# Optimization experiments

Measured on AMD Instinct MI355X. Metric: run time of the kernel, lower is better.

## Reference

```python
import jax, jax.numpy as jnp
import numpy as np
import math

B, S, D, H, L, V = 1, 2048, 512, 8, 2, 32000
DH = D // H
DFF = 2048
EPS = 1e-6
LN_EPS = 1e-5


def setup_inputs() -> dict:
    key = jax.random.key(0)
    ks = jax.random.split(key, 8)
    s = 0.02
    return {
        "input_ids": jax.random.randint(ks[0], (B, S), 0, V),
        "token_emb": jax.random.normal(ks[1], (V, D), jnp.float32) * s,
        "ln1_scale": jnp.ones((L, D), jnp.float32),
        "ln1_bias": jnp.zeros((L, D), jnp.float32),
        "qkv_w": jax.random.normal(ks[2], (L, D, 3 * D), jnp.float32) * s,
        "out_w": jax.random.normal(ks[3], (L, D, D), jnp.float32) * s,
        "ln2_scale": jnp.ones((L, D), jnp.float32),
        "ln2_bias": jnp.zeros((L, D), jnp.float32),
        "mlp_w1": jax.random.normal(ks[4], (L, D, DFF), jnp.float32) * s,
        "mlp_b1": jnp.zeros((L, DFF), jnp.float32),
        "mlp_w2": jax.random.normal(ks[5], (L, DFF, D), jnp.float32) * s,
        "mlp_b2": jnp.zeros((L, D), jnp.float32),
        "lnf_scale": jnp.ones((D,), jnp.float32),
        "lnf_bias": jnp.zeros((D,), jnp.float32),
        "head_w": jax.random.normal(ks[6], (D, V), jnp.float32) * s,
    }


def layernorm(x, scale, bias):
    mu = jnp.mean(x, axis=-1, keepdims=True)
    var = jnp.mean(jnp.square(x - mu), axis=-1, keepdims=True)
    return (x - mu) * jax.lax.rsqrt(var + LN_EPS) * scale + bias


def feature_map(x):
    return jax.nn.elu(x) + 1.0


def sinusoidal_pe(seq_len, d_model, dtype):
    pos = jnp.arange(seq_len, dtype=jnp.float32)[:, None]
    div = jnp.exp(jnp.arange(0, d_model, 2, dtype=jnp.float32) * (-math.log(10000.0) / d_model))
    pe = jnp.zeros((seq_len, d_model), jnp.float32)
    pe = pe.at[:, 0::2].set(jnp.sin(pos * div))
    pe = pe.at[:, 1::2].set(jnp.cos(pos * div))
    return pe.astype(dtype)


def linear_causal_attn(x, w_qkv, w_out):
    # x: (b, s, d)
    b, s, _ = x.shape
    qkv = x @ w_qkv  # (b, s, 3d)
    q, k, v = jnp.split(qkv, 3, axis=-1)
    split_heads = lambda t: t.reshape(b, s, H, DH).transpose(0, 2, 1, 3)  # (b,h,s,dh)
    q, k, v = split_heads(q), split_heads(k), split_heads(v)
    phi_q = feature_map(q)
    phi_k = feature_map(k)
    k_cum = jnp.cumsum(phi_k, axis=2)                          # (b,h,s,dh)
    kv = jnp.einsum('bhsi,bhsj->bhsij', phi_k, v)              # (b,h,s,dh,dh)
    kv_cum = jnp.cumsum(kv, axis=2)
    numer = jnp.einsum('bhsi,bhsij->bhsj', phi_q, kv_cum)      # (b,h,s,dh)
    denom = jnp.einsum('bhsi,bhsi->bhs', phi_q, k_cum) + EPS
    attn = numer / denom[..., None]
    attn = attn.transpose(0, 2, 1, 3).reshape(b, s, D)
    return attn @ w_out


def reference(input_ids, token_emb, ln1_scale, ln1_bias, qkv_w, out_w,
              ln2_scale, ln2_bias, mlp_w1, mlp_b1, mlp_w2, mlp_b2,
              lnf_scale, lnf_bias, head_w):
    tok = token_emb[input_ids]                 # (b, s, d)
    pos = sinusoidal_pe(input_ids.shape[1], D, tok.dtype)[None]
    x = tok + pos
    for l in range(L):
        a = linear_causal_attn(layernorm(x, ln1_scale[l], ln1_bias[l]), qkv_w[l], out_w[l])
        x = x + a
        h = layernorm(x, ln2_scale[l], ln2_bias[l])
        h = jax.nn.gelu(h @ mlp_w1[l] + mlp_b1[l], approximate=False) @ mlp_w2[l] + mlp_b2[l]
        x = x + h
    x = layernorm(x, lnf_scale, lnf_bias)
    logits = x @ head_w                        # (b, s, vocab)
    return logits
```

## Files before the change

### kernel.cpp

```cpp
#include <hip/hip_runtime.h>
#include <cstdint>

typedef unsigned short u16;
typedef __bf16 bf16x8 __attribute__((ext_vector_type(8)));
typedef float f32x4 __attribute__((ext_vector_type(4)));

#define DEV __device__ __forceinline__

DEV u16 f2bf(float f) {
  union { float f; unsigned u; } v; v.f = f;
  unsigned u = v.u;
  u += 0x7FFFu + ((u >> 16) & 1u);
  return (u16)(u >> 16);
}
DEV float bf2f(u16 u) {
  union { unsigned u; float f; } v; v.u = ((unsigned)u) << 16;
  return v.f;
}

DEV void load16(const u16* g, u16* l) {
  __builtin_amdgcn_global_load_lds(
      (const __attribute__((address_space(1))) unsigned int*)(const void*)g,
      (__attribute__((address_space(3))) unsigned int*)l, 16, 0, 0);
}

__global__ __launch_bounds__(256) void prep_kernel(
    const float* __restrict__ qkvw, const float* __restrict__ outw,
    const float* __restrict__ w1, const float* __restrict__ w2,
    const float* __restrict__ hw, u16* __restrict__ wq_t, u16* __restrict__ wo_t,
    u16* __restrict__ w1_t, u16* __restrict__ w2_t, u16* __restrict__ wh_t,
    const int* __restrict__ ids, const float* __restrict__ emb,
    const float* __restrict__ sc, const float* __restrict__ bi,
    float* __restrict__ x, u16* __restrict__ xn) {
  int b = blockIdx.x;
  __shared__ float t[64][65];
  if (b >= 5536) {
    int lane = threadIdx.x & 63, wave = threadIdx.x >> 6;
    int row = (b - 5536) * 4 + wave;
    int id = ids[row];
    float v[8];
#pragma unroll
    for (int i = 0; i < 8; ++i) {
      int c = lane + i * 64;
      float tk = emb[(size_t)id * 512 + c];
      int dp = c & ~1;
      float dv = expf((float)dp * (-9.210340371976184f / 512.0f));
      float ang = (float)row * dv;
      float pe = (c & 1) ? cosf(ang) : sinf(ang);
      v[i] = tk + pe;
      x[(size_t)row * 512 + c] = v[i];
    }
    float s = 0.f;
#pragma unroll
    for (int i = 0; i < 8; ++i) s += v[i];
#pragma unroll
    for (int m = 32; m; m >>= 1) s += __shfl_xor(s, m, 64);
    float mu = s * (1.0f / 512.0f);
    float var = 0.f;
#pragma unroll
    for (int i = 0; i < 8; ++i) { float d = v[i] - mu; var += d * d; }
#pragma unroll
    for (int m = 32; m; m >>= 1) var += __shfl_xor(var, m, 64);
    float rs = rsqrtf(var * (1.0f / 512.0f) + 1e-5f);
    u16* orow = xn + (size_t)row * 512;
#pragma unroll
    for (int i = 0; i < 8; ++i) {
      int c = lane + i * 64;
      orow[c] = f2bf((v[i] - mu) * rs * sc[c] + bi[c]);
    }
    return;
  }
  const float* in; u16* out; int K, N, nx, ky;
  if (b < 384)       { int z = b / 192, r = b % 192; nx = r % 24; ky = r / 24;
                       in = qkvw + (size_t)z * 786432; out = wq_t + (size_t)z * 786432; N = 1536; K = 512; }
  else if (b < 512)  { int tt = b - 384, z = tt / 64, r = tt % 64; nx = r % 8; ky = r / 8;
                       in = outw + (size_t)z * 262144; out = wo_t + (size_t)z * 262144; N = 512; K = 512; }
  else if (b < 1024) { int tt = b - 512, z = tt / 256, r = tt % 256; nx = r % 32; ky = r / 32;
                       in = w1 + (size_t)z * 1048576; out = w1_t + (size_t)z * 1048576; N = 2048; K = 512; }
  else if (b < 1536) { int tt = b - 1024, z = tt / 256, r = tt % 256; nx = r % 8; ky = r / 8;
                       in = w2 + (size_t)z * 1048576; out = w2_t + (size_t)z * 1048576; N = 512; K = 2048; }
  else               { int tt = b - 1536; nx = tt % 500; ky = tt / 500;
                       in = hw; out = wh_t; N = 32000; K = 512; }
  int n0 = nx * 64, k0 = ky * 64;
  for (int e = threadIdx.x; e < 4096; e += 256) {
    int r = e >> 6, c = e & 63;
    t[r][c] = in[(size_t)(k0 + r) * N + n0 + c];
  }
  __syncthreads();
  for (int e = threadIdx.x; e < 4096; e += 256) {
    int r = e >> 6, c = e & 63;
    out[(size_t)(n0 + r) * K + k0 + c] = f2bf(t[c][r]);
  }
}

__global__ __launch_bounds__(256) void reduce_ln(const float* __restrict__ part, int nz,
    const float* __restrict__ bias, float* __restrict__ x,
    const float* __restrict__ sc, const float* __restrict__ bi, u16* __restrict__ xn) {
  int lane = threadIdx.x & 63, wave = threadIdx.x >> 6;
  int row = blockIdx.x * 4 + wave;
  float* xr = x + (size_t)row * 512;
  float v[8];
#pragma unroll
  for (int i = 0; i < 8; ++i) v[i] = xr[lane + i * 64];
  if (bias) {
#pragma unroll
    for (int i = 0; i < 8; ++i) v[i] += bias[lane + i * 64];
  }
  for (int z = 0; z < nz; ++z) {
    const float* pz = part + (size_t)z * 1048576 + (size_t)row * 512;
#pragma unroll
    for (int i = 0; i < 8; ++i) v[i] += pz[lane + i * 64];
  }
#pragma unroll
  for (int i = 0; i < 8; ++i) xr[lane + i * 64] = v[i];
  float s = 0.f;
#pragma unroll
  for (int i = 0; i < 8; ++i) s += v[i];
#pragma unroll
  for (int m = 32; m; m >>= 1) s += __shfl_xor(s, m, 64);
  float mu = s * (1.0f / 512.0f);
  float var = 0.f;
#pragma unroll
  for (int i = 0; i < 8; ++i) { float d = v[i] - mu; var += d * d; }
#pragma unroll
  for (int m = 32; m; m >>= 1) var += __shfl_xor(var, m, 64);
  float rs = rsqrtf(var * (1.0f / 512.0f) + 1e-5f);
  u16* orow = xn + (size_t)row * 512;
#pragma unroll
  for (int i = 0; i < 8; ++i) {
    int c = lane + i * 64;
    orow[c] = f2bf((v[i] - mu) * rs * sc[c] + bi[c]);
  }
}

__global__ __launch_bounds__(256) void attn_intra(const u16* __restrict__ pq,
    const u16* __restrict__ pk, const u16* __restrict__ pv,
    float* __restrict__ numer, float* __restrict__ denom,
    float* __restrict__ KVc, float* __restrict__ Ksc) {
  int c = blockIdx.x, h = blockIdx.y;
  int s0 = c * 128;
  __shared__ u16 kl[128 * 72];
  __shared__ u16 vl[128 * 72];
  __shared__ u16 kT[64 * 136];
  __shared__ u16 vT[64 * 136];
  __shared__ u16 P[128 * 136];
  int tid = threadIdx.x, lane = tid & 63, w = tid >> 6;
  int fr = lane & 15, kb = lane >> 4, rg = lane >> 4;
  const size_t base = ((size_t)h * 2048 + s0) * 64;

  for (int e = tid; e < 1024; e += 256) {
    int r = e >> 3, c8 = (e & 7) * 8;
    *(bf16x8*)&kl[r * 72 + c8] = *(const bf16x8*)&pk[base + r * 64 + c8];
    *(bf16x8*)&vl[r * 72 + c8] = *(const bf16x8*)&pv[base + r * 64 + c8];
  }
  int fiA = w, fiB = 7 - w;
  const u16* qA = pq + base + (size_t)(fiA * 16 + fr) * 64 + kb * 8;
  const u16* qB = pq + base + (size_t)(fiB * 16 + fr) * 64 + kb * 8;
  bf16x8 aQ0a = *(const bf16x8*)qA, aQ1a = *(const bf16x8*)(qA + 32);
  bf16x8 aQ0b = *(const bf16x8*)qB, aQ1b = *(const bf16x8*)(qB + 32);
  __syncthreads();

  {
    int dh = tid & 63, sb = tid >> 6;
#pragma unroll
    for (int b8 = 0; b8 < 4; ++b8) {
      int sbase = sb * 32 + b8 * 8;
      u16 tk[8], tv[8];
#pragma unroll
      for (int j = 0; j < 8; ++j) {
        tk[j] = kl[(sbase + j) * 72 + dh];
        tv[j] = vl[(sbase + j) * 72 + dh];
      }
      *(int4*)&kT[dh * 136 + sbase] = *(const int4*)tk;
      *(int4*)&vT[dh * 136 + sbase] = *(const int4*)tv;
    }
  }

#pragma unroll
  for (int ph = 0; ph < 2; ++ph) {
    int fi = ph ? fiB : fiA;
    bf16x8 aQ0 = ph ? aQ0b : aQ0a, aQ1 = ph ? aQ1b : aQ1a;
    f32x4 dsum = {0.f, 0.f, 0.f, 0.f};
    for (int fj = 0; fj <= fi; ++fj) {
      f32x4 s4 = {0.f, 0.f, 0.f, 0.f};
      bf16x8 b0 = *(const bf16x8*)&kl[(fj * 16 + fr) * 72 + kb * 8];
      bf16x8 b1 = *(const bf16x8*)&kl[(fj * 16 + fr) * 72 + kb * 8 + 32];
      s4 = __builtin_amdgcn_mfma_f32_16x16x32_bf16(aQ0, b0, s4, 0, 0, 0);
      s4 = __builtin_amdgcn_mfma_f32_16x16x32_bf16(aQ1, b1, s4, 0, 0, 0);
      int colL = fj * 16 + fr;
#pragma unroll
      for (int rr = 0; rr < 4; ++rr) {
        int rowL = fi * 16 + rg * 4 + rr;
        float mv = (colL <= rowL) ? s4[rr] : 0.f;
        dsum[rr] += mv;
        P[rowL * 136 + colL] = f2bf(mv);
      }
    }
    if ((fi & 1) == 0) {
      int colL = (fi + 1) * 16 + fr;
#pragma unroll
      for (int rr = 0; rr < 4; ++rr) P[(fi * 16 + rg * 4 + rr) * 136 + colL] = 0;
    }
#pragma unroll
    for (int rr = 0; rr < 4; ++rr) {
      float v = dsum[rr];
      v += __shfl_xor(v, 1, 16); v += __shfl_xor(v, 2, 16);
      v += __shfl_xor(v, 4, 16); v += __shfl_xor(v, 8, 16);
      if (fr == 0) denom[(size_t)h * 2048 + s0 + fi * 16 + rg * 4 + rr] = v;
    }
  }
  __syncthreads();

#pragma unroll
  for (int ph = 0; ph < 2; ++ph) {
    int fi = ph ? fiB : fiA;
    int ktmax = (fi + 2) >> 1;
    f32x4 o0 = {0,0,0,0}, o1 = {0,0,0,0}, o2 = {0,0,0,0}, o3 = {0,0,0,0};
    for (int kt = 0; kt < ktmax; ++kt) {
      bf16x8 aP = *(const bf16x8*)&P[(fi * 16 + fr) * 136 + kt * 32 + kb * 8];
      o0 = __builtin_amdgcn_mfma_f32_16x16x32_bf16(aP, *(const bf16x8*)&vT[(0 * 16 + fr) * 136 + kt * 32 + kb * 8], o0, 0, 0, 0);
      o1 = __builtin_amdgcn_mfma_f32_16x16x32_bf16(aP, *(const bf16x8*)&vT[(1 * 16 + fr) * 136 + kt * 32 + kb * 8], o1, 0, 0, 0);
      o2 = __builtin_amdgcn_mfma_f32_16x16x32_bf16(aP, *(const bf16x8*)&vT[(2 * 16 + fr) * 136 + kt * 32 + kb * 8], o2, 0, 0, 0);
      o3 = __builtin_amdgcn_mfma_f32_16x16x32_bf16(aP, *(const bf16x8*)&vT[(3 * 16 + fr) * 136 + kt * 32 + kb * 8], o3, 0, 0, 0);
    }
#pragma unroll
    for (int rr = 0; rr < 4; ++rr) {
      size_t rb = base + (size_t)(fi * 16 + rg * 4 + rr) * 64;
      numer[rb + 0 + fr]  = o0[rr];
      numer[rb + 16 + fr] = o1[rr];
      numer[rb + 32 + fr] = o2[rr];
      numer[rb + 48 + fr] = o3[rr];
    }
  }

  {
    f32x4 k0 = {0,0,0,0}, k1 = {0,0,0,0}, k2 = {0,0,0,0}, k3 = {0,0,0,0};
    for (int kt = 0; kt < 4; ++kt) {
      bf16x8 aK = *(const bf16x8*)&kT[(w * 16 + fr) * 136 + kt * 32 + kb * 8];
      k0 = __builtin_amdgcn_mfma_f32_16x16x32_bf16(aK, *(const bf16x8*)&vT[(0 * 16 + fr) * 136 + kt * 32 + kb * 8], k0, 0, 0, 0);
      k1 = __builtin_amdgcn_mfma_f32_16x16x32_bf16(aK, *(const bf16x8*)&vT[(1 * 16 + fr) * 136 + kt * 32 + kb * 8], k1, 0, 0, 0);
      k2 = __builtin_amdgcn_mfma_f32_16x16x32_bf16(aK, *(const bf16x8*)&vT[(2 * 16 + fr) * 136 + kt * 32 + kb * 8], k2, 0, 0, 0);
      k3 = __builtin_amdgcn_mfma_f32_16x16x32_bf16(aK, *(const bf16x8*)&vT[(3 * 16 + fr) * 136 + kt * 32 + kb * 8], k3, 0, 0, 0);
    }
    float* kvb = KVc + ((size_t)h * 16 + c) * 4096;
#pragma unroll
    for (int rr = 0; rr < 4; ++rr) {
      int row = w * 16 + rg * 4 + rr;
      kvb[row * 64 + 0 + fr]  = k0[rr];
      kvb[row * 64 + 16 + fr] = k1[rr];
      kvb[row * 64 + 32 + fr] = k2[rr];
      kvb[row * 64 + 48 + fr] = k3[rr];
    }
  }
  if (tid < 64) {
    float s = 0.f;
    for (int t8 = 0; t8 < 16; ++t8) {
      bf16x8 kv = *(const bf16x8*)&kT[tid * 136 + t8 * 8];
#pragma unroll
      for (int tt = 0; tt < 8; ++tt) s += bf2f(((const u16*)&kv)[tt]);
    }
    Ksc[((size_t)h * 16 + c) * 64 + tid] = s;
  }
}

__global__ __launch_bounds__(256) void attn_inter(const u16* __restrict__ pq,
    const float* __restrict__ numer, const float* __restrict__ denom,
    const float* __restrict__ KVc, const float* __restrict__ Ksc,
    u16* __restrict__ attn) {
  int c = blockIdx.x, h = blockIdx.y;
  int s0 = c * 128;
  __shared__ float KVp[4096];
  __shared__ float Kp[64];
  __shared__ float ql[128 * 65];
  int tid = threadIdx.x;
  for (int e = tid; e < 1024; e += 256) {
    f32x4 a = {0.f, 0.f, 0.f, 0.f};
    for (int cp = 0; cp < c; ++cp)
      a += *(const f32x4*)&KVc[((size_t)h * 16 + cp) * 4096 + e * 4];
    *(f32x4*)&KVp[e * 4] = a;
  }
  if (tid < 64) {
    float a = 0.f;
    for (int cp = 0; cp < c; ++cp) a += Ksc[((size_t)h * 16 + cp) * 64 + tid];
    Kp[tid] = a;
  }
  for (int e = tid; e < 1024; e += 256) {
    bf16x8 q8 = *(const bf16x8*)&pq[((size_t)h * 2048 + s0) * 64 + e * 8];
    int row = e >> 3, cb = (e & 7) * 8;
#pragma unroll
    for (int tt = 0; tt < 8; ++tt) ql[row * 65 + cb + tt] = bf2f(((const u16*)&q8)[tt]);
  }
  __syncthreads();
  int s = tid >> 1, half = tid & 1;
  float num[32];
  {
    const float* np_ = numer + ((size_t)h * 2048 + s0 + s) * 64 + half * 32;
#pragma unroll
    for (int i = 0; i < 8; ++i) *(f32x4*)&num[i * 4] = *(const f32x4*)&np_[i * 4];
  }
  float den = denom[(size_t)h * 2048 + s0 + s] + 1e-6f;
  for (int i = 0; i < 64; ++i) {
    float qv = ql[s * 65 + i];
    den += qv * Kp[i];
    const f32x4* kv = (const f32x4*)&KVp[i * 64 + half * 32];
#pragma unroll
    for (int j4 = 0; j4 < 8; ++j4) {
      f32x4 kvv = kv[j4];
#pragma unroll
      for (int t = 0; t < 4; ++t) num[j4 * 4 + t] += qv * kvv[t];
    }
  }
  float inv = 1.f / den;
  u16* op = attn + (size_t)(s0 + s) * 512 + h * 64 + half * 32;
#pragma unroll
  for (int j = 0; j < 32; ++j) op[j] = f2bf(num[j] * inv);
}

template <int EPI>
__global__ __launch_bounds__(512, 2) void gemm_bt(const u16* __restrict__ A,
    const u16* __restrict__ B, float* __restrict__ outF, u16* __restrict__ outB,
    const float* __restrict__ bias, int M, int N, int K, int Ksplit) {
  __shared__ u16 lds[32768];
  int tid = threadIdx.x, lane = tid & 63, w = tid >> 6;
  int f = blockIdx.x + gridDim.x * blockIdx.y;
  int m0 = (f & 15) << 7, n0 = (f >> 4) << 7;
  int wr = w >> 2, wc = w & 3;
  int fr = lane & 15, kb = lane >> 4;
  int z = blockIdx.z;
  int kbeg = z * Ksplit;
  int KT = Ksplit >> 6;

  auto stage = [&](int d, int u, int k0) {
    int t = u & 1;
    int row = t * 64 + w * 8 + (lane >> 3);
    int slot = (lane & 7) ^ ((lane >> 3) & 7);
    const u16* g = (u < 2 ? A + (size_t)(m0 + row) * K : B + (size_t)(n0 + row) * K)
                   + k0 + slot * 8;
    int dst = (u < 2 ? d * 8192 : 16384 + d * 8192) + t * 4096 + w * 512;
    load16(g, &lds[dst]);
  };
  auto rdA = [&](int d, int i, int kk) {
    int row = wr * 64 + i * 16 + fr;
    return *(const bf16x8*)&lds[d * 8192 + row * 64 + ((((kk << 2) | kb) ^ (fr & 7)) << 3)];
  };
  auto rdB = [&](int d, int j, int kk) {
    int row = wc * 32 + j * 16 + fr;
    return *(const bf16x8*)&lds[16384 + d * 8192 + row * 64 + ((((kk << 2) | kb) ^ (fr & 7)) << 3)];
  };

  f32x4 acc[4][2];
#pragma unroll
  for (int i = 0; i < 4; ++i)
#pragma unroll
    for (int j = 0; j < 2; ++j) acc[i][j] = (f32x4){0.f, 0.f, 0.f, 0.f};

#pragma unroll 1
  for (int u = 0; u < 4; ++u) stage(0, u, kbeg);
  __syncthreads();

  for (int t = 0; t < KT; ++t) {
    int d = t & 1, e = d ^ 1;
    int k1 = kbeg + ((t + 1) << 6);
    bool pre = (t + 1) < KT;
    bf16x8 aF[4], bF[2];
    if (pre) { stage(e, 0, k1); stage(e, 1, k1); }
#pragma unroll
    for (int i = 0; i < 4; ++i) aF[i] = rdA(d, i, 0);
#pragma unroll
    for (int j = 0; j < 2; ++j) bF[j] = rdB(d, j, 0);
    __builtin_amdgcn_s_setprio(1);
#pragma unroll
    for (int i = 0; i < 4; ++i)
#pragma unroll
      for (int j = 0; j < 2; ++j)
        acc[i][j] = __builtin_amdgcn_mfma_f32_16x16x32_bf16(aF[i], bF[j], acc[i][j], 0, 0, 0);
    __builtin_amdgcn_s_setprio(0);
    __builtin_amdgcn_sched_barrier(0);
    if (pre) { stage(e, 2, k1); stage(e, 3, k1); }
#pragma unroll
    for (int i = 0; i < 4; ++i) aF[i] = rdA(d, i, 1);
#pragma unroll
    for (int j = 0; j < 2; ++j) bF[j] = rdB(d, j, 1);
    __builtin_amdgcn_s_setprio(1);
#pragma unroll
    for (int i = 0; i < 4; ++i)
#pragma unroll
      for (int j = 0; j < 2; ++j)
        acc[i][j] = __builtin_amdgcn_mfma_f32_16x16x32_bf16(aF[i], bF[j], acc[i][j], 0, 0, 0);
    __builtin_amdgcn_s_setprio(0);
    __syncthreads();
  }

  int rq = lane >> 4;
#pragma unroll
  for (int i = 0; i < 4; ++i) {
#pragma unroll
    for (int j = 0; j < 2; ++j) {
      int col = n0 + wc * 32 + j * 16 + fr;
#pragma unroll
      for (int r = 0; r < 4; ++r) {
        int row = m0 + wr * 64 + i * 16 + rq * 4 + r;
        size_t o = (size_t)row * N + col;
        float vacc = acc[i][j][r];
        if (EPI == 2) {
          float t = vacc + bias[col];
          outB[o] = f2bf(0.5f * t * (1.f + erff(t * 0.70710678118654752f)));
        } else if (EPI == 4) {
          int part = col >> 9, d = col & 511, h = d >> 6, dh = d & 63;
          float wv = (part == 2) ? vacc : (vacc > 0.f ? vacc + 1.f : expf(vacc));
          outB[(size_t)part * 1048576 + (((size_t)h * 2048 + row) * 64 + dh)] = f2bf(wv);
        } else {
          outF[(size_t)z * 1048576 + o] = vacc;
        }
      }
    }
  }
}

__global__ __launch_bounds__(512, 2) void gemm256(const u16* __restrict__ A,
    const u16* __restrict__ B, float* __restrict__ C, int M, int N, int K) {
  __shared__ u16 lds[65536];
  int tid = threadIdx.x, lane = tid & 63, w = tid >> 6;
  int f = blockIdx.x;
  {
    int nwg = gridDim.x;
    int q = nwg >> 3;
    f = (f & 7) * q + (f >> 3);
  }
  int m0 = (f & 7) << 8;
  int n0 = (f >> 3) << 8;
  int wr = w >> 2, wc = w & 3;
  int fr = lane & 15, kb = lane >> 4;

  auto stage = [&](int d, int u, int k0) {
    int us = u & 3;
    int row = us * 64 + w * 8 + (lane >> 3);
    int slot = (lane & 7) ^ ((lane >> 3) & 7);
    const u16* g = (u < 4 ? A + (size_t)(m0 + row) * K : B + (size_t)(n0 + row) * K)
                   + k0 + slot * 8;
    int dst = (u < 4 ? d * 16384 : 32768 + d * 16384) + us * 4096 + w * 512;
    load16(g, &lds[dst]);
  };
  auto rdA = [&](int d, int i, int kk) {
    int row = wr * 128 + i * 16 + fr;
    return *(const bf16x8*)&lds[d * 16384 + row * 64 + ((((kk << 2) | kb) ^ (fr & 7)) << 3)];
  };
  auto rdB = [&](int d, int j, int kk) {
    int row = wc * 64 + j * 16 + fr;
    return *(const bf16x8*)&lds[32768 + d * 16384 + row * 64 + ((((kk << 2) | kb) ^ (fr & 7)) << 3)];
  };

  f32x4 acc[8][4];
#pragma unroll
  for (int i = 0; i < 8; ++i)
#pragma unroll
    for (int j = 0; j < 4; ++j) acc[i][j] = (f32x4){0.f, 0.f, 0.f, 0.f};

  int KT = K >> 6;
#pragma unroll 1
  for (int u = 0; u < 8; ++u) stage(0, u, 0);
  __syncthreads();

  for (int t = 0; t < KT; ++t) {
    int d = t & 1, e = d ^ 1;
    int k1 = (t + 1) << 6;
    bool pre = (t + 1) < KT;
    bf16x8 aF[4][2], bF[4][2];
    if (pre) { stage(e, 0, k1); stage(e, 1, k1); }
// ... 56 lines not shown
#pragma unroll
    for (int j = 0; j < 4; ++j) {
      int col = n0 + wc * 64 + j * 16 + fr;
#pragma unroll
      for (int r = 0; r < 4; ++r) {
        int row = m0 + wr * 128 + i * 16 + rq * 4 + r;
        C[(size_t)row * N + col] = acc[i][j][r];
      }
    }
  }
}

extern "C" void kernel_launch(void* const* d_in, const int* in_sizes, int n_in,
                              void* d_out, int out_size, void* d_ws, size_t ws_size,
                              hipStream_t stream) {
  const int*   ids  = (const int*)d_in[0];
  const float* tok  = (const float*)d_in[1];
  const float* ln1s = (const float*)d_in[2];
  const float* ln1b = (const float*)d_in[3];
  const float* qkvw = (const float*)d_in[4];
  const float* outw = (const float*)d_in[5];
  const float* ln2s = (const float*)d_in[6];
  const float* ln2b = (const float*)d_in[7];
  const float* w1   = (const float*)d_in[8];
  const float* b1   = (const float*)d_in[9];
  const float* w2   = (const float*)d_in[10];
  const float* b2   = (const float*)d_in[11];
  const float* lnfs = (const float*)d_in[12];
  const float* lnfb = (const float*)d_in[13];
  const float* hw   = (const float*)d_in[14];
  float* out = (float*)d_out;

  char* ws = (char*)d_ws;
  size_t off = 0;
  auto carve = [&](size_t bytes) {
    char* p = ws + off;
    off = (off + bytes + 255) & ~(size_t)255;
    return p;
  };
  u16*   wq_t   = (u16*)carve(2ull * 1536 * 512 * 2);
  u16*   wo_t   = (u16*)carve(2ull * 512 * 512 * 2);
  u16*   w1_t   = (u16*)carve(2ull * 2048 * 512 * 2);
  u16*   w2_t   = (u16*)carve(2ull * 512 * 2048 * 2);
  u16*   wh_t   = (u16*)carve(32000ull * 512 * 2);
  float* x      = (float*)carve(2048ull * 512 * 4);
  u16*   xn     = (u16*)carve(2048ull * 512 * 2);
  u16*   phiAll = (u16*)carve(3ull * 8 * 2048 * 64 * 2);
  float* numer  = (float*)carve(8ull * 2048 * 64 * 4);
  float* denom  = (float*)carve(8ull * 2048 * 4);
  float* KVc    = (float*)carve(8ull * 16 * 4096 * 4);
  float* Ksc    = (float*)carve(8ull * 16 * 64 * 4);
  u16*   attn   = (u16*)carve(2048ull * 512 * 2);
  u16*   hmid   = (u16*)carve(2048ull * 2048 * 2);
  float* part   = (float*)carve(4ull * 2048 * 512 * 4);
  (void)ws_size; (void)in_sizes; (void)n_in; (void)out_size;

  u16* phiq = phiAll;
  u16* phik = phiAll + 1048576;
  u16* vbf  = phiAll + 2097152;

  prep_kernel<<<6048, 256, 0, stream>>>(qkvw, outw, w1, w2, hw,
                                        wq_t, wo_t, w1_t, w2_t, wh_t,
                                        ids, tok, ln1s, ln1b, x, xn);

  for (int l = 0; l < 2; ++l) {
    const u16* wq_l = wq_t + (size_t)l * 1536 * 512;
    const u16* wo_l = wo_t + (size_t)l * 512 * 512;
    const u16* w1_l = w1_t + (size_t)l * 2048 * 512;
    const u16* w2_l = w2_t + (size_t)l * 512 * 2048;
    const float* nls = (l == 0) ? ln1s + 512 : lnfs;
    const float* nlb = (l == 0) ? ln1b + 512 : lnfb;

    gemm_bt<4><<<dim3(12, 16), 512, 0, stream>>>(xn, wq_l, nullptr, phiAll, nullptr,
                                                 2048, 1536, 512, 512);
    attn_intra<<<dim3(16, 8), 256, 0, stream>>>(phiq, phik, vbf, numer, denom, KVc, Ksc);
    attn_inter<<<dim3(16, 8), 256, 0, stream>>>(phiq, numer, denom, KVc, Ksc, attn);
    gemm_bt<5><<<dim3(4, 16, 2), 512, 0, stream>>>(attn, wo_l, part, nullptr, nullptr,
                                                   2048, 512, 512, 256);
    reduce_ln<<<512, 256, 0, stream>>>(part, 2, nullptr, x, ln2s + l * 512, ln2b + l * 512, xn);
    gemm_bt<2><<<dim3(16, 16), 512, 0, stream>>>(xn, w1_l, nullptr, hmid, b1 + l * 2048,
                                                 2048, 2048, 512, 512);
    gemm_bt<5><<<dim3(4, 16, 4), 512, 0, stream>>>(hmid, w2_l, part, nullptr, nullptr,
                                                   2048, 512, 2048, 512);
    reduce_ln<<<512, 256, 0, stream>>>(part, 4, b2 + l * 512, x, nls, nlb, xn);
  }

  gemm256<<<1000, 512, 0, stream>>>(xn, wh_t, out, 2048, 32000, 512);
}
```

Measured before the change: 308.3 us.

## Fuse per-layer kernels into one cooperative persistent megakernel with grid syncs

Replaces the sixteen per-layer launches (QKV GEMM, attention intra/inter, out-proj, reduce+LN, MLP GEMMs) with a single cooperative kernel of 256 blocks of 512 threads. Stages are separated by grid.sync() calls. The attention and layernorm stages are remapped to 512-thread blocks with a different per-wave work split. This is meant to cut launch overhead and inter-kernel gaps. In exchange, many blocks sit idle in stages that use only 128 or 192 blocks, occupancy drops to one block per CU, and each stage now pays a grid-wide barrier.

```diff
diff --git a/kernel.cpp b/kernel.cpp
--- a/kernel.cpp
+++ b/kernel.cpp
@@ -1,5 +1,8 @@
 #include <hip/hip_runtime.h>
+#include <hip/hip_cooperative_groups.h>
 #include <cstdint>
+
+namespace cg = cooperative_groups;
 
 typedef unsigned short u16;
 typedef __bf16 bf16x8 __attribute__((ext_vector_type(8)));
@@ -93,240 +96,15 @@
   }
 }
 
-__global__ __launch_bounds__(256) void reduce_ln(const float* __restrict__ part, int nz,
-    const float* __restrict__ bias, float* __restrict__ x,
-    const float* __restrict__ sc, const float* __restrict__ bi, u16* __restrict__ xn) {
-  int lane = threadIdx.x & 63, wave = threadIdx.x >> 6;
-  int row = blockIdx.x * 4 + wave;
-  float* xr = x + (size_t)row * 512;
-  float v[8];
-#pragma unroll
-  for (int i = 0; i < 8; ++i) v[i] = xr[lane + i * 64];
-  if (bias) {
-#pragma unroll
-    for (int i = 0; i < 8; ++i) v[i] += bias[lane + i * 64];
-  }
-  for (int z = 0; z < nz; ++z) {
-    const float* pz = part + (size_t)z * 1048576 + (size_t)row * 512;
-#pragma unroll
-    for (int i = 0; i < 8; ++i) v[i] += pz[lane + i * 64];
-  }
-#pragma unroll
-  for (int i = 0; i < 8; ++i) xr[lane + i * 64] = v[i];
-  float s = 0.f;
-#pragma unroll
-  for (int i = 0; i < 8; ++i) s += v[i];
-#pragma unroll
-  for (int m = 32; m; m >>= 1) s += __shfl_xor(s, m, 64);
-  float mu = s * (1.0f / 512.0f);
-  float var = 0.f;
-#pragma unroll
-  for (int i = 0; i < 8; ++i) { float d = v[i] - mu; var += d * d; }
-#pragma unroll
-  for (int m = 32; m; m >>= 1) var += __shfl_xor(var, m, 64);
-  float rs = rsqrtf(var * (1.0f / 512.0f) + 1e-5f);
-  u16* orow = xn + (size_t)row * 512;
-#pragma unroll
-  for (int i = 0; i < 8; ++i) {
-    int c = lane + i * 64;
-    orow[c] = f2bf((v[i] - mu) * rs * sc[c] + bi[c]);
-  }
-}
-
-__global__ __launch_bounds__(256) void attn_intra(const u16* __restrict__ pq,
-    const u16* __restrict__ pk, const u16* __restrict__ pv,
-    float* __restrict__ numer, float* __restrict__ denom,
-    float* __restrict__ KVc, float* __restrict__ Ksc) {
-  int c = blockIdx.x, h = blockIdx.y;
-  int s0 = c * 128;
-  __shared__ u16 kl[128 * 72];
-  __shared__ u16 vl[128 * 72];
-  __shared__ u16 kT[64 * 136];
-  __shared__ u16 vT[64 * 136];
-  __shared__ u16 P[128 * 136];
+
+template <int EPI>
+DEV void gemm_stage(u16* ldsp, int f, int z, const u16* A, const u16* B,
+                    float* outF, u16* outB, const float* bias,
+                    int N, int K, int Ksplit) {
   int tid = threadIdx.x, lane = tid & 63, w = tid >> 6;
-  int fr = lane & 15, kb = lane >> 4, rg = lane >> 4;
-  const size_t base = ((size_t)h * 2048 + s0) * 64;
-
-  for (int e = tid; e < 1024; e += 256) {
-    int r = e >> 3, c8 = (e & 7) * 8;
-    *(bf16x8*)&kl[r * 72 + c8] = *(const bf16x8*)&pk[base + r * 64 + c8];
-    *(bf16x8*)&vl[r * 72 + c8] = *(const bf16x8*)&pv[base + r * 64 + c8];
-  }
-  int fiA = w, fiB = 7 - w;
-  const u16* qA = pq + base + (size_t)(fiA * 16 + fr) * 64 + kb * 8;
-  const u16* qB = pq + base + (size_t)(fiB * 16 + fr) * 64 + kb * 8;
-  bf16x8 aQ0a = *(const bf16x8*)qA, aQ1a = *(const bf16x8*)(qA + 32);
-  bf16x8 aQ0b = *(const bf16x8*)qB, aQ1b = *(const bf16x8*)(qB + 32);
-  __syncthreads();
-
-  {
-    int dh = tid & 63, sb = tid >> 6;
-#pragma unroll
-    for (int b8 = 0; b8 < 4; ++b8) {
-      int sbase = sb * 32 + b8 * 8;
-      u16 tk[8], tv[8];
-#pragma unroll
-      for (int j = 0; j < 8; ++j) {
-        tk[j] = kl[(sbase + j) * 72 + dh];
-        tv[j] = vl[(sbase + j) * 72 + dh];
-      }
-      *(int4*)&kT[dh * 136 + sbase] = *(const int4*)tk;
-      *(int4*)&vT[dh * 136 + sbase] = *(const int4*)tv;
-    }
-  }
-
-#pragma unroll
-  for (int ph = 0; ph < 2; ++ph) {
-    int fi = ph ? fiB : fiA;
-    bf16x8 aQ0 = ph ? aQ0b : aQ0a, aQ1 = ph ? aQ1b : aQ1a;
-    f32x4 dsum = {0.f, 0.f, 0.f, 0.f};
-    for (int fj = 0; fj <= fi; ++fj) {
-      f32x4 s4 = {0.f, 0.f, 0.f, 0.f};
-      bf16x8 b0 = *(const bf16x8*)&kl[(fj * 16 + fr) * 72 + kb * 8];
-      bf16x8 b1 = *(const bf16x8*)&kl[(fj * 16 + fr) * 72 + kb * 8 + 32];
-      s4 = __builtin_amdgcn_mfma_f32_16x16x32_bf16(aQ0, b0, s4, 0, 0, 0);
-      s4 = __builtin_amdgcn_mfma_f32_16x16x32_bf16(aQ1, b1, s4, 0, 0, 0);
-      int colL = fj * 16 + fr;
-#pragma unroll
-      for (int rr = 0; rr < 4; ++rr) {
-        int rowL = fi * 16 + rg * 4 + rr;
-        float mv = (colL <= rowL) ? s4[rr] : 0.f;
-        dsum[rr] += mv;
-        P[rowL * 136 + colL] = f2bf(mv);
-      }
-    }
-    if ((fi & 1) == 0) {
-      int colL = (fi + 1) * 16 + fr;
-#pragma unroll
-      for (int rr = 0; rr < 4; ++rr) P[(fi * 16 + rg * 4 + rr) * 136 + colL] = 0;
-    }
-#pragma unroll
-    for (int rr = 0; rr < 4; ++rr) {
-      float v = dsum[rr];
-      v += __shfl_xor(v, 1, 16); v += __shfl_xor(v, 2, 16);
-      v += __shfl_xor(v, 4, 16); v += __shfl_xor(v, 8, 16);
-      if (fr == 0) denom[(size_t)h * 2048 + s0 + fi * 16 + rg * 4 + rr] = v;
-    }
-  }
-  __syncthreads();
-
-#pragma unroll
-  for (int ph = 0; ph < 2; ++ph) {
-    int fi = ph ? fiB : fiA;
-    int ktmax = (fi + 2) >> 1;
-    f32x4 o0 = {0,0,0,0}, o1 = {0,0,0,0}, o2 = {0,0,0,0}, o3 = {0,0,0,0};
-    for (int kt = 0; kt < ktmax; ++kt) {
-      bf16x8 aP = *(const bf16x8*)&P[(fi * 16 + fr) * 136 + kt * 32 + kb * 8];
-      o0 = __builtin_amdgcn_mfma_f32_16x16x32_bf16(aP, *(const bf16x8*)&vT[(0 * 16 + fr) * 136 + kt * 32 + kb * 8], o0, 0, 0, 0);
-      o1 = __builtin_amdgcn_mfma_f32_16x16x32_bf16(aP, *(const bf16x8*)&vT[(1 * 16 + fr) * 136 + kt * 32 + kb * 8], o1, 0, 0, 0);
-      o2 = __builtin_amdgcn_mfma_f32_16x16x32_bf16(aP, *(const bf16x8*)&vT[(2 * 16 + fr) * 136 + kt * 32 + kb * 8], o2, 0, 0, 0);
-      o3 = __builtin_amdgcn_mfma_f32_16x16x32_bf16(aP, *(const bf16x8*)&vT[(3 * 16 + fr) * 136 + kt * 32 + kb * 8], o3, 0, 0, 0);
-    }
-#pragma unroll
-    for (int rr = 0; rr < 4; ++rr) {
-      size_t rb = base + (size_t)(fi * 16 + rg * 4 + rr) * 64;
-      numer[rb + 0 + fr]  = o0[rr];
-      numer[rb + 16 + fr] = o1[rr];
-      numer[rb + 32 + fr] = o2[rr];
-      numer[rb + 48 + fr] = o3[rr];
-    }
-  }
-
-  {
-    f32x4 k0 = {0,0,0,0}, k1 = {0,0,0,0}, k2 = {0,0,0,0}, k3 = {0,0,0,0};
-    for (int kt = 0; kt < 4; ++kt) {
-      bf16x8 aK = *(const bf16x8*)&kT[(w * 16 + fr) * 136 + kt * 32 + kb * 8];
-      k0 = __builtin_amdgcn_mfma_f32_16x16x32_bf16(aK, *(const bf16x8*)&vT[(0 * 16 + fr) * 136 + kt * 32 + kb * 8], k0, 0, 0, 0);
-      k1 = __builtin_amdgcn_mfma_f32_16x16x32_bf16(aK, *(const bf16x8*)&vT[(1 * 16 + fr) * 136 + kt * 32 + kb * 8], k1, 0, 0, 0);
-      k2 = __builtin_amdgcn_mfma_f32_16x16x32_bf16(aK, *(const bf16x8*)&vT[(2 * 16 + fr) * 136 + kt * 32 + kb * 8], k2, 0, 0, 0);
-      k3 = __builtin_amdgcn_mfma_f32_16x16x32_bf16(aK, *(const bf16x8*)&vT[(3 * 16 + fr) * 136 + kt * 32 + kb * 8], k3, 0, 0, 0);
-    }
-    float* kvb = KVc + ((size_t)h * 16 + c) * 4096;
-#pragma unroll
-    for (int rr = 0; rr < 4; ++rr) {
-      int row = w * 16 + rg * 4 + rr;
-      kvb[row * 64 + 0 + fr]  = k0[rr];
-      kvb[row * 64 + 16 + fr] = k1[rr];
-      kvb[row * 64 + 32 + fr] = k2[rr];
-      kvb[row * 64 + 48 + fr] = k3[rr];
-    }
-  }
-  if (tid < 64) {
-    float s = 0.f;
-    for (int t8 = 0; t8 < 16; ++t8) {
-      bf16x8 kv = *(const bf16x8*)&kT[tid * 136 + t8 * 8];
-#pragma unroll
-      for (int tt = 0; tt < 8; ++tt) s += bf2f(((const u16*)&kv)[tt]);
-    }
-    Ksc[((size_t)h * 16 + c) * 64 + tid] = s;
-  }
-}
-
-__global__ __launch_bounds__(256) void attn_inter(const u16* __restrict__ pq,
-    const float* __restrict__ numer, const float* __restrict__ denom,
-    const float* __restrict__ KVc, const float* __restrict__ Ksc,
-    u16* __restrict__ attn) {
-  int c = blockIdx.x, h = blockIdx.y;
-  int s0 = c * 128;
-  __shared__ float KVp[4096];
-  __shared__ float Kp[64];
-  __shared__ float ql[128 * 65];
-  int tid = threadIdx.x;
-  for (int e = tid; e < 1024; e += 256) {
-    f32x4 a = {0.f, 0.f, 0.f, 0.f};
-    for (int cp = 0; cp < c; ++cp)
-      a += *(const f32x4*)&KVc[((size_t)h * 16 + cp) * 4096 + e * 4];
-    *(f32x4*)&KVp[e * 4] = a;
-  }
-  if (tid < 64) {
-    float a = 0.f;
-    for (int cp = 0; cp < c; ++cp) a += Ksc[((size_t)h * 16 + cp) * 64 + tid];
-    Kp[tid] = a;
-  }
-  for (int e = tid; e < 1024; e += 256) {
-    bf16x8 q8 = *(const bf16x8*)&pq[((size_t)h * 2048 + s0) * 64 + e * 8];
-    int row = e >> 3, cb = (e & 7) * 8;
-#pragma unroll
-    for (int tt = 0; tt < 8; ++tt) ql[row * 65 + cb + tt] = bf2f(((const u16*)&q8)[tt]);
-  }
-  __syncthreads();
-  int s = tid >> 1, half = tid & 1;
-  float num[32];
-  {
-    const float* np_ = numer + ((size_t)h * 2048 + s0 + s) * 64 + half * 32;
-#pragma unroll
-    for (int i = 0; i < 8; ++i) *(f32x4*)&num[i * 4] = *(const f32x4*)&np_[i * 4];
-  }
-  float den = denom[(size_t)h * 2048 + s0 + s] + 1e-6f;
-  for (int i = 0; i < 64; ++i) {
-    float qv = ql[s * 65 + i];
-    den += qv * Kp[i];
-    const f32x4* kv = (const f32x4*)&KVp[i * 64 + half * 32];
-#pragma unroll
-    for (int j4 = 0; j4 < 8; ++j4) {
-      f32x4 kvv = kv[j4];
-#pragma unroll
-      for (int t = 0; t < 4; ++t) num[j4 * 4 + t] += qv * kvv[t];
-    }
-  }
-  float inv = 1.f / den;
-  u16* op = attn + (size_t)(s0 + s) * 512 + h * 64 + half * 32;
-#pragma unroll
-  for (int j = 0; j < 32; ++j) op[j] = f2bf(num[j] * inv);
-}
-
-template <int EPI>
-__global__ __launch_bounds__(512, 2) void gemm_bt(const u16* __restrict__ A,
-    const u16* __restrict__ B, float* __restrict__ outF, u16* __restrict__ outB,
-    const float* __restrict__ bias, int M, int N, int K, int Ksplit) {
-  __shared__ u16 lds[32768];
-  int tid = threadIdx.x, lane = tid & 63, w = tid >> 6;
-  int f = blockIdx.x + gridDim.x * blockIdx.y;
   int m0 = (f & 15) << 7, n0 = (f >> 4) << 7;
   int wr = w >> 2, wc = w & 3;
   int fr = lane & 15, kb = lane >> 4;
-  int z = blockIdx.z;
   int kbeg = z * Ksplit;
   int KT = Ksplit >> 6;
 
@@ -337,15 +115,15 @@
     const u16* g = (u < 2 ? A + (size_t)(m0 + row) * K : B + (size_t)(n0 + row) * K)
                    + k0 + slot * 8;
     int dst = (u < 2 ? d * 8192 : 16384 + d * 8192) + t * 4096 + w * 512;
-    load16(g, &lds[dst]);
+    load16(g, &ldsp[dst]);
   };
   auto rdA = [&](int d, int i, int kk) {
     int row = wr * 64 + i * 16 + fr;
-    return *(const bf16x8*)&lds[d * 8192 + row * 64 + ((((kk << 2) | kb) ^ (fr & 7)) << 3)];
+    return *(const bf16x8*)&ldsp[d * 8192 + row * 64 + ((((kk << 2) | kb) ^ (fr & 7)) << 3)];
   };
   auto rdB = [&](int d, int j, int kk) {
     int row = wc * 32 + j * 16 + fr;
-    return *(const bf16x8*)&lds[16384 + d * 8192 + row * 64 + ((((kk << 2) | kb) ^ (fr & 7)) << 3)];
+    return *(const bf16x8*)&ldsp[16384 + d * 8192 + row * 64 + ((((kk << 2) | kb) ^ (fr & 7)) << 3)];
   };
 
   f32x4 acc[4][2];
@@ -414,6 +192,267 @@
         }
       }
     }
+  }
+}
+
+DEV void attn_intra_stage(u16* smem, int bid, const u16* pq, const u16* pk,
+    const u16* pv, float* numer, float* denom, float* KVc, float* Ksc) {
+  int c = bid & 15, h = bid >> 4;
+  int s0 = c * 128;
+  u16* kl = smem;
+  u16* vl = smem + 9216;
+  u16* kT = smem + 18432;
+  u16* vT = smem + 27136;
+  u16* P  = smem + 35840;
+  int tid = threadIdx.x, lane = tid & 63, w = tid >> 6;
+  int fr = lane & 15, kb = lane >> 4, rg = lane >> 4;
+  const size_t base = ((size_t)h * 2048 + s0) * 64;
+
+  for (int e = tid; e < 1024; e += 512) {
+    int r = e >> 3, c8 = (e & 7) * 8;
+    *(bf16x8*)&kl[r * 72 + c8] = *(const bf16x8*)&pk[base + r * 64 + c8];
+    *(bf16x8*)&vl[r * 72 + c8] = *(const bf16x8*)&pv[base + r * 64 + c8];
+  }
+  int fi = w;
+  const u16* qA = pq + base + (size_t)(fi * 16 + fr) * 64 + kb * 8;
+  bf16x8 aQ0 = *(const bf16x8*)qA, aQ1 = *(const bf16x8*)(qA + 32);
+  __syncthreads();
+
+  {
+    int dh = tid & 63, sb = tid >> 6;
+#pragma unroll
+    for (int b8 = 0; b8 < 2; ++b8) {
+      int sbase = sb * 16 + b8 * 8;
+      u16 tk[8], tv[8];
+#pragma unroll
+      for (int j = 0; j < 8; ++j) {
+        tk[j] = kl[(sbase + j) * 72 + dh];
+        tv[j] = vl[(sbase + j) * 72 + dh];
+      }
+      *(int4*)&kT[dh * 136 + sbase] = *(const int4*)tk;
+      *(int4*)&vT[dh * 136 + sbase] = *(const int4*)tv;
+    }
+  }
+
+  {
+    f32x4 dsum = {0.f, 0.f, 0.f, 0.f};
+    for (int fj = 0; fj <= fi; ++fj) {
+      f32x4 s4 = {0.f, 0.f, 0.f, 0.f};
+      bf16x8 b0 = *(const bf16x8*)&kl[(fj * 16 + fr) * 72 + kb * 8];
+      bf16x8 b1 = *(const bf16x8*)&kl[(fj * 16 + fr) * 72 + kb * 8 + 32];
+      s4 = __builtin_amdgcn_mfma_f32_16x16x32_bf16(aQ0, b0, s4, 0, 0, 0);
+      s4 = __builtin_amdgcn_mfma_f32_16x16x32_bf16(aQ1, b1, s4, 0, 0, 0);
+      int colL = fj * 16 + fr;
+#pragma unroll
+      for (int rr = 0; rr < 4; ++rr) {
+        int rowL = fi * 16 + rg * 4 + rr;
+        float mv = (colL <= rowL) ? s4[rr] : 0.f;
+        dsum[rr] += mv;
+        P[rowL * 136 + colL] = f2bf(mv);
+      }
+    }
+    if ((fi & 1) == 0) {
+      int colL = (fi + 1) * 16 + fr;
+#pragma unroll
+      for (int rr = 0; rr < 4; ++rr) P[(fi * 16 + rg * 4 + rr) * 136 + colL] = 0;
+    }
+#pragma unroll
+    for (int rr = 0; rr < 4; ++rr) {
+      float v = dsum[rr];
+      v += __shfl_xor(v, 1, 16); v += __shfl_xor(v, 2, 16);
+      v += __shfl_xor(v, 4, 16); v += __shfl_xor(v, 8, 16);
+      if (fr == 0) denom[(size_t)h * 2048 + s0 + fi * 16 + rg * 4 + rr] = v;
+    }
+  }
+  __syncthreads();
+
+  {
+    int ktmax = (fi + 2) >> 1;
+    f32x4 o0 = {0,0,0,0}, o1 = {0,0,0,0}, o2 = {0,0,0,0}, o3 = {0,0,0,0};
+    for (int kt = 0; kt < ktmax; ++kt) {
+      bf16x8 aP = *(const bf16x8*)&P[(fi * 16 + fr) * 136 + kt * 32 + kb * 8];
+      o0 = __builtin_amdgcn_mfma_f32_16x16x32_bf16(aP, *(const bf16x8*)&vT[(0 * 16 + fr) * 136 + kt * 32 + kb * 8], o0, 0, 0, 0);
+      o1 = __builtin_amdgcn_mfma_f32_16x16x32_bf16(aP, *(const bf16x8*)&vT[(1 * 16 + fr) * 136 + kt * 32 + kb * 8], o1, 0, 0, 0);
+      o2 = __builtin_amdgcn_mfma_f32_16x16x32_bf16(aP, *(const bf16x8*)&vT[(2 * 16 + fr) * 136 + kt * 32 + kb * 8], o2, 0, 0, 0);
+      o3 = __builtin_amdgcn_mfma_f32_16x16x32_bf16(aP, *(const bf16x8*)&vT[(3 * 16 + fr) * 136 + kt * 32 + kb * 8], o3, 0, 0, 0);
+    }
+#pragma unroll
+    for (int rr = 0; rr < 4; ++rr) {
+      size_t rb = base + (size_t)(fi * 16 + rg * 4 + rr) * 64;
+      numer[rb + 0 + fr]  = o0[rr];
+      numer[rb + 16 + fr] = o1[rr];
+      numer[rb + 32 + fr] = o2[rr];
+      numer[rb + 48 + fr] = o3[rr];
+    }
+  }
+
+  if (w < 4) {
+    f32x4 k0 = {0,0,0,0}, k1 = {0,0,0,0}, k2 = {0,0,0,0}, k3 = {0,0,0,0};
+    for (int kt = 0; kt < 4; ++kt) {
+      bf16x8 aK = *(const bf16x8*)&kT[(w * 16 + fr) * 136 + kt * 32 + kb * 8];
+      k0 = __builtin_amdgcn_mfma_f32_16x16x32_bf16(aK, *(const bf16x8*)&vT[(0 * 16 + fr) * 136 + kt * 32 + kb * 8], k0, 0, 0, 0);
+      k1 = __builtin_amdgcn_mfma_f32_16x16x32_bf16(aK, *(const bf16x8*)&vT[(1 * 16 + fr) * 136 + kt * 32 + kb * 8], k1, 0, 0, 0);
+      k2 = __builtin_amdgcn_mfma_f32_16x16x32_bf16(aK, *(const bf16x8*)&vT[(2 * 16 + fr) * 136 + kt * 32 + kb * 8], k2, 0, 0, 0);
+      k3 = __builtin_amdgcn_mfma_f32_16x16x32_bf16(aK, *(const bf16x8*)&vT[(3 * 16 + fr) * 136 + kt * 32 + kb * 8], k3, 0, 0, 0);
+    }
+    float* kvb = KVc + ((size_t)h * 16 + c) * 4096;
+#pragma unroll
+    for (int rr = 0; rr < 4; ++rr) {
+      int row = w * 16 + rg * 4 + rr;
+      kvb[row * 64 + 0 + fr]  = k0[rr];
+      kvb[row * 64 + 16 + fr] = k1[rr];
+      kvb[row * 64 + 32 + fr] = k2[rr];
+      kvb[row * 64 + 48 + fr] = k3[rr];
+    }
+  } else if (w == 4) {
+    float s = 0.f;
+    for (int t8 = 0; t8 < 16; ++t8) {
+      bf16x8 kv = *(const bf16x8*)&kT[lane * 136 + t8 * 8];
+#pragma unroll
+      for (int tt = 0; tt < 8; ++tt) s += bf2f(((const u16*)&kv)[tt]);
+    }
+    Ksc[((size_t)h * 16 + c) * 64 + lane] = s;
+  }
+}
+
+DEV void attn_inter_stage(u16* smem, int bid, const u16* pq,
+    const float* numer, const float* denom, const float* KVc,
+    const float* Ksc, u16* attn) {
+  int c = bid & 15, h = bid >> 4;
+  int s0 = c * 128;
+  float* KVp = (float*)smem;
+  float* Kp  = KVp + 4096;
+  float* ql  = KVp + 4160;
+  int tid = threadIdx.x;
+  for (int e = tid; e < 1024; e += 512) {
+    f32x4 a = {0.f, 0.f, 0.f, 0.f};
+    for (int cp = 0; cp < c; ++cp)
+      a += *(const f32x4*)&KVc[((size_t)h * 16 + cp) * 4096 + e * 4];
+    *(f32x4*)&KVp[e * 4] = a;
+  }
+  if (tid < 64) {
+    float a = 0.f;
+    for (int cp = 0; cp < c; ++cp) a += Ksc[((size_t)h * 16 + cp) * 64 + tid];
+    Kp[tid] = a;
+  }
+  for (int e = tid; e < 1024; e += 512) {
+    bf16x8 q8 = *(const bf16x8*)&pq[((size_t)h * 2048 + s0) * 64 + e * 8];
+    int row = e >> 3, cb = (e & 7) * 8;
+#pragma unroll
+    for (int tt = 0; tt < 8; ++tt) ql[row * 65 + cb + tt] = bf2f(((const u16*)&q8)[tt]);
+  }
+  __syncthreads();
+  int s = tid >> 2, q = tid & 3;
+  float num[16];
+  {
+    const float* np_ = numer + ((size_t)h * 2048 + s0 + s) * 64 + q * 16;
+#pragma unroll
+    for (int i = 0; i < 4; ++i) *(f32x4*)&num[i * 4] = *(const f32x4*)&np_[i * 4];
+  }
+  float den = denom[(size_t)h * 2048 + s0 + s] + 1e-6f;
+  for (int i = 0; i < 64; ++i) {
+    float qv = ql[s * 65 + i];
+    den += qv * Kp[i];
+    const f32x4* kv = (const f32x4*)&KVp[i * 64 + q * 16];
+#pragma unroll
+    for (int j4 = 0; j4 < 4; ++j4) {
+      f32x4 kvv = kv[j4];
+#pragma unroll
+      for (int t = 0; t < 4; ++t) num[j4 * 4 + t] += qv * kvv[t];
+    }
+  }
+  float inv = 1.f / den;
+  u16* op = attn + (size_t)(s0 + s) * 512 + h * 64 + q * 16;
+#pragma unroll
+  for (int j = 0; j < 16; ++j) op[j] = f2bf(num[j] * inv);
+}
+
+DEV void reduce_ln_stage(int bid, const float* part, int nz, const float* bias,
+    float* x, const float* sc, const float* bi, u16* xn) {
+  int lane = threadIdx.x & 63, wave = threadIdx.x >> 6;
+  int row = bid * 8 + wave;
+  float* xr = x + (size_t)row * 512;
+  float v[8];
+#pragma unroll
+  for (int i = 0; i < 8; ++i) v[i] = xr[lane + i * 64];
+  if (bias) {
+#pragma unroll
+    for (int i = 0; i < 8; ++i) v[i] += bias[lane + i * 64];
+  }
+  for (int z = 0; z < nz; ++z) {
+    const float* pz = part + (size_t)z * 1048576 + (size_t)row * 512;
+#pragma unroll
+    for (int i = 0; i < 8; ++i) v[i] += pz[lane + i * 64];
+  }
+#pragma unroll
+  for (int i = 0; i < 8; ++i) xr[lane + i * 64] = v[i];
+  float s = 0.f;
+#pragma unroll
+  for (int i = 0; i < 8; ++i) s += v[i];
+#pragma unroll
+  for (int m = 32; m; m >>= 1) s += __shfl_xor(s, m, 64);
+  float mu = s * (1.0f / 512.0f);
+  float var = 0.f;
+#pragma unroll
+  for (int i = 0; i < 8; ++i) { float d = v[i] - mu; var += d * d; }
+#pragma unroll
+  for (int m = 32; m; m >>= 1) var += __shfl_xor(var, m, 64);
+  float rs = rsqrtf(var * (1.0f / 512.0f) + 1e-5f);
+  u16* orow = xn + (size_t)row * 512;
+#pragma unroll
+  for (int i = 0; i < 8; ++i) {
+    int c = lane + i * 64;
+    orow[c] = f2bf((v[i] - mu) * rs * sc[c] + bi[c]);
+  }
+}
+
+struct MegaArgs {
+  const float *ln1s, *ln1b, *ln2s, *ln2b, *lnfs, *lnfb, *b1, *b2;
+  const u16 *wq_t, *wo_t, *w1_t, *w2_t;
+  float* x; u16* xn; u16* phiAll;
+  float *numer, *denom, *KVc, *Ksc;
+  u16 *attn, *hmid; float* part;
+};
+
+__global__ __launch_bounds__(512, 1) void mega_kernel(MegaArgs a) {
+  cg::grid_group grid = cg::this_grid();
+  __shared__ __align__(16) u16 smem[53248];
+  int bid = blockIdx.x;
+
+  u16* phiq = a.phiAll;
+  u16* phik = a.phiAll + 1048576;
+  u16* vbf  = a.phiAll + 2097152;
+
+  for (int l = 0; l < 2; ++l) {
+    const u16* wq_l = a.wq_t + (size_t)l * 1536 * 512;
+    const u16* wo_l = a.wo_t + (size_t)l * 512 * 512;
+    const u16* w1_l = a.w1_t + (size_t)l * 2048 * 512;
+    const u16* w2_l = a.w2_t + (size_t)l * 512 * 2048;
+
+    if (bid < 192)
+      gemm_stage<4>(smem, bid, 0, a.xn, wq_l, nullptr, a.phiAll, nullptr, 1536, 512, 512);
+    grid.sync();
+    if (bid < 128)
+      attn_intra_stage(smem, bid, phiq, phik, vbf, a.numer, a.denom, a.KVc, a.Ksc);
+    grid.sync();
+    if (bid < 128)
+      attn_inter_stage(smem, bid, phiq, a.numer, a.denom, a.KVc, a.Ksc, a.attn);
+    grid.sync();
+    if (bid < 128)
+      gemm_stage<5>(smem, bid & 63, bid >> 6, a.attn, wo_l, a.part, nullptr, nullptr,
+                    512, 512, 256);
+    grid.sync();
+    reduce_ln_stage(bid, a.part, 2, nullptr, a.x, a.ln2s + l * 512, a.ln2b + l * 512, a.xn);
+    grid.sync();
+    gemm_stage<2>(smem, bid, 0, a.xn, w1_l, nullptr, a.hmid, a.b1 + l * 2048, 2048, 512, 512);
+    grid.sync();
+    gemm_stage<5>(smem, bid & 63, bid >> 6, a.hmid, w2_l, a.part, nullptr, nullptr,
+                  512, 2048, 512);
+    grid.sync();
+    const float* nls = (l == 0) ? a.ln1s + 512 : a.lnfs;
+    const float* nlb = (l == 0) ? a.ln1b + 512 : a.lnfb;
+    reduce_ln_stage(bid, a.part, 4, a.b2 + l * 512, a.x, nls, nlb, a.xn);
+    grid.sync();
   }
 }
 
@@ -579,35 +618,20 @@
   float* part   = (float*)carve(4ull * 2048 * 512 * 4);
   (void)ws_size; (void)in_sizes; (void)n_in; (void)out_size;
 
-  u16* phiq = phiAll;
-  u16* phik = phiAll + 1048576;
-  u16* vbf  = phiAll + 2097152;
-
   prep_kernel<<<6048, 256, 0, stream>>>(qkvw, outw, w1, w2, hw,
                                         wq_t, wo_t, w1_t, w2_t, wh_t,
                                         ids, tok, ln1s, ln1b, x, xn);
 
-  for (int l = 0; l < 2; ++l) {
-    const u16* wq_l = wq_t + (size_t)l * 1536 * 512;
-    const u16* wo_l = wo_t + (size_t)l * 512 * 512;
-    const u16* w1_l = w1_t + (size_t)l * 2048 * 512;
-    const u16* w2_l = w2_t + (size_t)l * 512 * 2048;
-    const float* nls = (l == 0) ? ln1s + 512 : lnfs;
-    const float* nlb = (l == 0) ? ln1b + 512 : lnfb;
-
-    gemm_bt<4><<<dim3(12, 16), 512, 0, stream>>>(xn, wq_l, nullptr, phiAll, nullptr,
-                                                 2048, 1536, 512, 512);
-    attn_intra<<<dim3(16, 8), 256, 0, stream>>>(phiq, phik, vbf, numer, denom, KVc, Ksc);
-    attn_inter<<<dim3(16, 8), 256, 0, stream>>>(phiq, numer, denom, KVc, Ksc, attn);
-    gemm_bt<5><<<dim3(4, 16, 2), 512, 0, stream>>>(attn, wo_l, part, nullptr, nullptr,
-                                                   2048, 512, 512, 256);
-    reduce_ln<<<512, 256, 0, stream>>>(part, 2, nullptr, x, ln2s + l * 512, ln2b + l * 512, xn);
-    gemm_bt<2><<<dim3(16, 16), 512, 0, stream>>>(xn, w1_l, nullptr, hmid, b1 + l * 2048,
-                                                 2048, 2048, 512, 512);
-    gemm_bt<5><<<dim3(4, 16, 4), 512, 0, stream>>>(hmid, w2_l, part, nullptr, nullptr,
-                                                   2048, 512, 2048, 512);
-    reduce_ln<<<512, 256, 0, stream>>>(part, 4, b2 + l * 512, x, nls, nlb, xn);
-  }
+  MegaArgs ma;
+  ma.ln1s = ln1s; ma.ln1b = ln1b; ma.ln2s = ln2s; ma.ln2b = ln2b;
+  ma.lnfs = lnfs; ma.lnfb = lnfb; ma.b1 = b1; ma.b2 = b2;
+  ma.wq_t = wq_t; ma.wo_t = wo_t; ma.w1_t = w1_t; ma.w2_t = w2_t;
+  ma.x = x; ma.xn = xn; ma.phiAll = phiAll;
+  ma.numer = numer; ma.denom = denom; ma.KVc = KVc; ma.Ksc = Ksc;
+  ma.attn = attn; ma.hmid = hmid; ma.part = part;
+  void* kargs[] = { &ma };
+  hipLaunchCooperativeKernel(reinterpret_cast<void*>(mega_kernel),
+                             dim3(256), dim3(512), kargs, 0, stream);
 
   gemm256<<<1000, 512, 0, stream>>>(xn, wh_t, out, 2048, 32000, 512);
 }
```

Result: slower. 849.2 us (+175.5%).

## Drop split-K partials; accumulate residual and bias directly in GEMM epilogue

Applied to the files above, without the earlier changes.

Removes the split-K partial buffer for the attention output and MLP down-projection GEMMs. Each GEMM now runs the full K loop and adds its result (plus optional bias) into the residual stream x in its epilogue. The reduce+layernorm kernel becomes a pure layernorm. This saves the partial-buffer writes and reads but cuts grid size to 64 blocks, reducing parallelism on a many-CU GPU.

```diff
diff --git a/kernel.cpp b/kernel.cpp
--- a/kernel.cpp
+++ b/kernel.cpp
@@ -93,26 +93,14 @@
   }
 }
 
-__global__ __launch_bounds__(256) void reduce_ln(const float* __restrict__ part, int nz,
-    const float* __restrict__ bias, float* __restrict__ x,
+__global__ __launch_bounds__(256) void ln_kernel(const float* __restrict__ x,
     const float* __restrict__ sc, const float* __restrict__ bi, u16* __restrict__ xn) {
   int lane = threadIdx.x & 63, wave = threadIdx.x >> 6;
   int row = blockIdx.x * 4 + wave;
-  float* xr = x + (size_t)row * 512;
+  const float* xr = x + (size_t)row * 512;
   float v[8];
 #pragma unroll
   for (int i = 0; i < 8; ++i) v[i] = xr[lane + i * 64];
-  if (bias) {
-#pragma unroll
-    for (int i = 0; i < 8; ++i) v[i] += bias[lane + i * 64];
-  }
-  for (int z = 0; z < nz; ++z) {
-    const float* pz = part + (size_t)z * 1048576 + (size_t)row * 512;
-#pragma unroll
-    for (int i = 0; i < 8; ++i) v[i] += pz[lane + i * 64];
-  }
-#pragma unroll
-  for (int i = 0; i < 8; ++i) xr[lane + i * 64] = v[i];
   float s = 0.f;
 #pragma unroll
   for (int i = 0; i < 8; ++i) s += v[i];
@@ -319,16 +307,14 @@
 template <int EPI>
 __global__ __launch_bounds__(512, 2) void gemm_bt(const u16* __restrict__ A,
     const u16* __restrict__ B, float* __restrict__ outF, u16* __restrict__ outB,
-    const float* __restrict__ bias, int M, int N, int K, int Ksplit) {
+    const float* __restrict__ bias, int M, int N, int K) {
   __shared__ u16 lds[32768];
   int tid = threadIdx.x, lane = tid & 63, w = tid >> 6;
   int f = blockIdx.x + gridDim.x * blockIdx.y;
   int m0 = (f & 15) << 7, n0 = (f >> 4) << 7;
   int wr = w >> 2, wc = w & 3;
   int fr = lane & 15, kb = lane >> 4;
-  int z = blockIdx.z;
-  int kbeg = z * Ksplit;
-  int KT = Ksplit >> 6;
+  int KT = K >> 6;
 
   auto stage = [&](int d, int u, int k0) {
     int t = u & 1;
@@ -355,12 +341,12 @@
     for (int j = 0; j < 2; ++j) acc[i][j] = (f32x4){0.f, 0.f, 0.f, 0.f};
 
 #pragma unroll 1
-  for (int u = 0; u < 4; ++u) stage(0, u, kbeg);
+  for (int u = 0; u < 4; ++u) stage(0, u, 0);
   __syncthreads();
 
   for (int t = 0; t < KT; ++t) {
     int d = t & 1, e = d ^ 1;
-    int k1 = kbeg + ((t + 1) << 6);
+    int k1 = (t + 1) << 6;
     bool pre = (t + 1) < KT;
     bf16x8 aF[4], bF[2];
     if (pre) { stage(e, 0, k1); stage(e, 1, k1); }
@@ -410,7 +396,9 @@
           float wv = (part == 2) ? vacc : (vacc > 0.f ? vacc + 1.f : expf(vacc));
           outB[(size_t)part * 1048576 + (((size_t)h * 2048 + row) * 64 + dh)] = f2bf(wv);
         } else {
-          outF[(size_t)z * 1048576 + o] = vacc;
+          float add = vacc;
+          if (bias) add += bias[col];
+          outF[o] += add;
         }
       }
     }
@@ -576,7 +564,6 @@
   float* Ksc    = (float*)carve(8ull * 16 * 64 * 4);
   u16*   attn   = (u16*)carve(2048ull * 512 * 2);
   u16*   hmid   = (u16*)carve(2048ull * 2048 * 2);
-  float* part   = (float*)carve(4ull * 2048 * 512 * 4);
   (void)ws_size; (void)in_sizes; (void)n_in; (void)out_size;
 
   u16* phiq = phiAll;
@@ -596,17 +583,17 @@
     const float* nlb = (l == 0) ? ln1b + 512 : lnfb;
 
     gemm_bt<4><<<dim3(12, 16), 512, 0, stream>>>(xn, wq_l, nullptr, phiAll, nullptr,
-                                                 2048, 1536, 512, 512);
+                                                 2048, 1536, 512);
     attn_intra<<<dim3(16, 8), 256, 0, stream>>>(phiq, phik, vbf, numer, denom, KVc, Ksc);
     attn_inter<<<dim3(16, 8), 256, 0, stream>>>(phiq, numer, denom, KVc, Ksc, attn);
-    gemm_bt<5><<<dim3(4, 16, 2), 512, 0, stream>>>(attn, wo_l, part, nullptr, nullptr,
-                                                   2048, 512, 512, 256);
-    reduce_ln<<<512, 256, 0, stream>>>(part, 2, nullptr, x, ln2s + l * 512, ln2b + l * 512, xn);
+    gemm_bt<6><<<dim3(4, 16), 512, 0, stream>>>(attn, wo_l, x, nullptr, nullptr,
+                                                2048, 512, 512);
+    ln_kernel<<<512, 256, 0, stream>>>(x, ln2s + l * 512, ln2b + l * 512, xn);
     gemm_bt<2><<<dim3(16, 16), 512, 0, stream>>>(xn, w1_l, nullptr, hmid, b1 + l * 2048,
-                                                 2048, 2048, 512, 512);
-    gemm_bt<5><<<dim3(4, 16, 4), 512, 0, stream>>>(hmid, w2_l, part, nullptr, nullptr,
-                                                   2048, 512, 2048, 512);
-    reduce_ln<<<512, 256, 0, stream>>>(part, 4, b2 + l * 512, x, nls, nlb, xn);
+                                                 2048, 2048, 512);
+    gemm_bt<6><<<dim3(4, 16), 512, 0, stream>>>(hmid, w2_l, x, nullptr, b2 + l * 512,
+                                                2048, 512, 2048);
+    ln_kernel<<<512, 256, 0, stream>>>(x, nls, nlb, xn);
   }
 
   gemm256<<<1000, 512, 0, stream>>>(xn, wh_t, out, 2048, 32000, 512);
```

After: 359.1 us. 1.17x slower.
